# Optimization experiments

Measured on AMD Instinct MI355X. Metric: run time of the kernel, lower is better.

## Reference

```python
import jax, jax.numpy as jnp
import numpy as np

N_NODES = 50000
N_EDGES = 800000
N_INPUT = 512
N_HIDDEN = 64


def setup_inputs() -> dict:
    key = jax.random.key(0)
    ks = jax.random.split(key, 6)
    x = jax.random.normal(ks[0], (1, N_NODES, N_INPUT), dtype=jnp.float32)
    edge_rows = jax.random.randint(ks[1], (N_EDGES,), 0, N_NODES, dtype=jnp.int64)
    edge_cols = jax.random.randint(ks[2], (N_EDGES,), 0, N_NODES, dtype=jnp.int64)
    edge_vals = jax.random.uniform(ks[3], (N_EDGES,), dtype=jnp.float32)
    # xavier_normal_ on fc.weight: std = sqrt(2 / (fan_in + fan_out))
    std = float(np.sqrt(2.0 / (N_INPUT + N_HIDDEN)))
    W = jax.random.normal(ks[4], (N_HIDDEN, N_INPUT), dtype=jnp.float32) * std
    b = jnp.zeros((N_HIDDEN,), dtype=jnp.float32)
    alpha = jnp.full((1,), 0.25, dtype=jnp.float32)  # PReLU default init
    return {"x": x, "edge_rows": edge_rows, "edge_cols": edge_cols,
            "edge_vals": edge_vals, "W": W, "b": b, "alpha": alpha}


def reference(x, edge_rows, edge_cols, edge_vals, W, b, alpha):
    # Linear projection: [1, N, F_in] @ [F_in, F_out] -> [1, N, F_out]
    h = jnp.einsum('bnf,hf->bnh', x, W) + b
    h = jnp.squeeze(h, 0)  # [N, F_out]
    # spmm(adj, h): out[i] = sum_e vals[e] * h[cols[e]] for rows[e] == i
    msgs = edge_vals[:, None] * h[edge_cols]  # [E, F_out]
    agg = jax.ops.segment_sum(msgs, edge_rows, num_segments=N_NODES)  # [N, F_out]
    out = agg[None, :, :]  # [1, N, F_out]
    # PReLU with shared alpha
    return jnp.where(out >= 0, out, alpha * out)
```

## Files before the change

kernel.cpp:

```cpp
#include <hip/hip_runtime.h>

#define NODES 50000
#define NEDGES 800000
#define NIN 512
#define NHID 64

#define NB 391
#define BCAP 2560
#define EB 4096
#define NBA 196

#define XSTR 268

typedef __attribute__((ext_vector_type(8))) short short8v;
typedef __attribute__((ext_vector_type(8))) unsigned short ushort8v;
typedef __attribute__((ext_vector_type(4))) float f32x4;
typedef __attribute__((ext_vector_type(4))) unsigned int uint4v;

#define H_OFF    0
#define WBF_OFF  1600000
#define GCUR_OFF 1616384
#define RMETA_OFF 1616896
#define ECV2_OFF 1716896

__device__ inline unsigned short f2bf(float f) {
  unsigned u = __builtin_bit_cast(unsigned, f);
  u += 0x7FFF + ((u >> 16) & 1);
  return (unsigned short)(u >> 16);
}
__device__ inline float bf2f(unsigned short u) {
  return __builtin_bit_cast(float, (unsigned)u << 16);
}

__global__ __launch_bounds__(256) void init_kernel(
    const float* __restrict__ W, unsigned int* __restrict__ wbf,
    int* __restrict__ gcur)
{
  int i = blockIdx.x * 256 + threadIdx.x;
  if (i < NIN * NHID / 2) {
    float2 w = reinterpret_cast<const float2*>(W)[i];
    wbf[i] = (unsigned)f2bf(w.x) | ((unsigned)f2bf(w.y) << 16);
  }
  if (i < NB) gcur[i] = 0;
}

__global__ __launch_bounds__(256) void binA_kernel(
    const int* __restrict__ rows, const int* __restrict__ cols,
    const float* __restrict__ vals, int* __restrict__ gcur,
    int2* __restrict__ ecv2)
{
  __shared__ int hist[NB];
  __shared__ unsigned short slots[EB];
  int bid = blockIdx.x;
  int tid = (int)threadIdx.x;
  int e0 = bid * EB;

  for (int i = tid; i < NB; i += 256) hist[i] = 0;
  __syncthreads();
  #pragma unroll 4
  for (int k = 0; k < EB / 256; ++k) {
    int i = e0 + k * 256 + tid;
    if (i < NEDGES) {
      int r = rows[i];
      int s = atomicAdd(&hist[r >> 7], 1);
      slots[k * 256 + tid] = (unsigned short)s;
    }
  }
  __syncthreads();
  for (int i = tid; i < NB; i += 256) {
    int c = hist[i];
    hist[i] = c ? atomicAdd(&gcur[i], c) : 0;
  }
  __syncthreads();
  #pragma unroll 4
  for (int k = 0; k < EB / 256; ++k) {
    int i = e0 + k * 256 + tid;
    if (i < NEDGES) {
      int r = rows[i];
      int bkt = r >> 7;
      int sl = hist[bkt] + (int)slots[k * 256 + tid];
      if (sl < BCAP)
        ecv2[(long)bkt * BCAP + sl] =
            make_int2(cols[i] | ((r & 127) << 17), __float_as_int(vals[i]));
    }
  }
}

__global__ __launch_bounds__(256) void gemm_kernel(
    const float* __restrict__ x, const unsigned short* __restrict__ wbf,
    const float* __restrict__ b, unsigned short* __restrict__ h)
{
  __shared__ unsigned int xls[64 * XSTR];
  int blk = blockIdx.x;
  int tid = (int)threadIdx.x;

  #pragma unroll 8
  for (int c = 0; c < 32; ++c) {
    int idx = c * 256 + tid;
    int lrow = idx >> 7;
    int k4 = idx & 127;
    long grow = (long)blk * 64 + lrow;
    if (grow >= NODES) grow = NODES - 1;
    float4 v = *reinterpret_cast<const float4*>(x + grow * NIN + k4 * 4);
    unsigned lo, hi;
    asm("v_cvt_pk_bf16_f32 %0, %1, %2" : "=v"(lo) : "v"(v.x), "v"(v.y));
    asm("v_cvt_pk_bf16_f32 %0, %1, %2" : "=v"(hi) : "v"(v.z), "v"(v.w));
    *reinterpret_cast<uint2*>(&xls[lrow * XSTR + k4 * 2]) = make_uint2(lo, hi);
  }
  __syncthreads();

  int wv = tid >> 6;
  int lane = tid & 63;
  int r16 = lane & 15;
  int kg  = lane >> 4;
  int lrow = wv * 16 + r16;
  const unsigned int* rowp = &xls[lrow * XSTR];
  const unsigned short* wp = wbf + (long)r16 * NIN + kg * 8;

  f32x4 acc[4] = {{0,0,0,0},{0,0,0,0},{0,0,0,0},{0,0,0,0}};

  #pragma unroll
  for (int m = 0; m < 16; ++m) {
    uint4v ap = *reinterpret_cast<const uint4v*>(rowp + m * 16 + kg * 4);
    short8v af = __builtin_bit_cast(short8v, ap);
    #pragma unroll
    for (int ft = 0; ft < 4; ++ft) {
      short8v bfr = *reinterpret_cast<const short8v*>(
          wp + (long)ft * 16 * NIN + m * 32);
      acc[ft] = __builtin_amdgcn_mfma_f32_16x16x32_bf16(af, bfr, acc[ft], 0, 0, 0);
    }
  }

  int nbase = blk * 64 + wv * 16 + kg * 4;
  #pragma unroll
  for (int ft = 0; ft < 4; ++ft) {
    float bias = b[ft * 16 + r16];
    #pragma unroll
    for (int r = 0; r < 4; ++r) {
      int node = nbase + r;
      if (node < NODES)
        h[(long)node * NHID + ft * 16 + r16] = f2bf(acc[ft][r] + bias);
    }
  }
}

__global__ __launch_bounds__(256) void sortb_kernel(
    const int* __restrict__ gcur, int2* __restrict__ ecv2,
    int2* __restrict__ rowmeta)
{
  __shared__ int2 ed[BCAP];
  __shared__ unsigned short slots[BCAP];
  __shared__ int hist[128], base[128], stmp[128];
  int bkt = blockIdx.x;
  int tid = (int)threadIdx.x;

  int n = gcur[bkt];
  if (n > BCAP) n = BCAP;
  int2* bptr = ecv2 + (long)bkt * BCAP;

  if (tid < 128) hist[tid] = 0;
  __syncthreads();

  for (int i = tid; i < n; i += 256) {
    int2 e = bptr[i];
    ed[i] = e;
    int rl = e.x >> 17;
    slots[i] = (unsigned short)atomicAdd(&hist[rl], 1);
  }
  __syncthreads();

  int v = (tid < 128) ? hist[tid] : 0;
  if (tid < 128) stmp[tid] = v;
  __syncthreads();
  for (int d = 1; d < 128; d <<= 1) {
    int t = (tid < 128 && tid >= d) ? stmp[tid - d] : 0;
    __syncthreads();
    if (tid < 128) stmp[tid] += t;
    __syncthreads();
  }
  if (tid < 128) base[tid] = stmp[tid] - v;
  __syncthreads();

  for (int i = tid; i < n; i += 256) {
    int2 e = ed[i];
    int rl = e.x >> 17;
    int pos = base[rl] + (int)slots[i];
    bptr[pos] = make_int2(e.x & 0x1FFFF, e.y);
  }

  if (tid < 128) {
    int row = bkt * 128 + tid;
    if (row < NODES)
      rowmeta[row] = make_int2(bkt * BCAP + base[tid], hist[tid]);
  }
}

__global__ __launch_bounds__(256) void gather_kernel(
    const int2* __restrict__ rowmeta, const int2* __restrict__ ecv2,
    const unsigned short* __restrict__ h, const float* __restrict__ alpha,
    float* __restrict__ out)
{
  int wid = (int)((blockIdx.x * 256 + threadIdx.x) >> 6);
  if (wid >= NODES) return;
  int lane = (int)(threadIdx.x & 63);
  int eg = lane >> 3;
  int fo = lane & 7;
  int2 m = rowmeta[wid];
  int deg = m.y;
  const int2* base = ecv2 + m.x;
  float a = alpha[0];

  float acc[8] = {0.f, 0.f, 0.f, 0.f, 0.f, 0.f, 0.f, 0.f};
  int j = eg;
  int2 e = (j < deg) ? base[j] : make_int2(0, 0);
  while (j < deg) {
    int2 en = (j + 8 < deg) ? base[j + 8] : make_int2(0, 0);
    float v = __int_as_float(e.y);
    ushort8v hv = *reinterpret_cast<const ushort8v*>(&h[(long)e.x * NHID + fo * 8]);
    #pragma unroll
    for (int k = 0; k < 8; ++k)
      acc[k] = fmaf(v, bf2f(hv[k]), acc[k]);
    e = en;
    j += 8;
  }

  #pragma unroll
  for (int k = 0; k < 8; ++k) {
    acc[k] += __shfl_xor(acc[k], 8);
    acc[k] += __shfl_xor(acc[k], 16);
    acc[k] += __shfl_xor(acc[k], 32);
  }

  if (eg == 0) {
    float4 o0, o1;
    o0.x = acc[0] >= 0.f ? acc[0] : a * acc[0];
    o0.y = acc[1] >= 0.f ? acc[1] : a * acc[1];
    o0.z = acc[2] >= 0.f ? acc[2] : a * acc[2];
    o0.w = acc[3] >= 0.f ? acc[3] : a * acc[3];
    o1.x = acc[4] >= 0.f ? acc[4] : a * acc[4];
    o1.y = acc[5] >= 0.f ? acc[5] : a * acc[5];
    o1.z = acc[6] >= 0.f ? acc[6] : a * acc[6];
    o1.w = acc[7] >= 0.f ? acc[7] : a * acc[7];
    *reinterpret_cast<float4*>(&out[(long)wid * NHID + fo * 8]) = o0;
    *reinterpret_cast<float4*>(&out[(long)wid * NHID + fo * 8 + 4]) = o1;
  }
}

extern "C" void kernel_launch(void* const* d_in, const int* in_sizes, int n_in,
                              void* d_out, int out_size, void* d_ws, size_t ws_size,
                              hipStream_t stream) {
  const float* x     = (const float*)d_in[0];
  const int*   rows  = (const int*)d_in[1];
  const int*   cols  = (const int*)d_in[2];
  const float* vals  = (const float*)d_in[3];
  const float* W     = (const float*)d_in[4];
  const float* b     = (const float*)d_in[5];
  const float* alpha = (const float*)d_in[6];
  float* out = (float*)d_out;

  float* wsf = (float*)d_ws;
  unsigned short* h     = (unsigned short*)(wsf + H_OFF);
  unsigned int*   wbf   = (unsigned int*)(wsf + WBF_OFF);
  int*            gcur  = (int*)(wsf + GCUR_OFF);
  int2*           rmeta = (int2*)(wsf + RMETA_OFF);
  int2*           ecv2  = (int2*)(wsf + ECV2_OFF);

  init_kernel<<<64, 256, 0, stream>>>(W, wbf, gcur);
  binA_kernel<<<NBA, 256, 0, stream>>>(rows, cols, vals, gcur, ecv2);
  gemm_kernel<<<(NODES + 63) / 64, 256, 0, stream>>>(
      x, (const unsigned short*)wbf, b, h);
  sortb_kernel<<<NB, 256, 0, stream>>>(gcur, ecv2, rmeta);
  gather_kernel<<<NODES * 64 / 256, 256, 0, stream>>>(rmeta, ecv2, h, alpha, out);
}
```

Baseline: 107.1 us.

## Split GEMM K across waves with direct global loads and LDS reduction

The GEMM no longer stages a 64-row bf16 tile of x in LDS. Each 512-thread block now covers 32 rows, and its 8 waves split the K dimension four ways. Each wave loads x straight from global memory into registers, converts it to bf16 and feeds MFMA. Partial sums are reduced through a small LDS buffer before adding bias and storing. This removes the serial stage-then-compute barrier and raises parallelism, but adds an LDS reduction and uses narrower, less coalesced 32-byte-per-lane global reads.

```diff
diff --git a/kernel.cpp b/kernel.cpp
--- a/kernel.cpp
+++ b/kernel.cpp
@@ -9,8 +9,6 @@
 #define BCAP 2560
 #define EB 4096
 #define NBA 196
-
-#define XSTR 268
 
 typedef __attribute__((ext_vector_type(8))) short short8v;
 typedef __attribute__((ext_vector_type(8))) unsigned short ushort8v;
@@ -86,61 +84,69 @@
   }
 }
 
-__global__ __launch_bounds__(256) void gemm_kernel(
+__global__ __launch_bounds__(512) void gemm_kernel(
     const float* __restrict__ x, const unsigned short* __restrict__ wbf,
     const float* __restrict__ b, unsigned short* __restrict__ h)
 {
-  __shared__ unsigned int xls[64 * XSTR];
+  __shared__ float red[8][64][18];
   int blk = blockIdx.x;
   int tid = (int)threadIdx.x;
-
-  #pragma unroll 8
-  for (int c = 0; c < 32; ++c) {
-    int idx = c * 256 + tid;
-    int lrow = idx >> 7;
-    int k4 = idx & 127;
-    long grow = (long)blk * 64 + lrow;
-    if (grow >= NODES) grow = NODES - 1;
-    float4 v = *reinterpret_cast<const float4*>(x + grow * NIN + k4 * 4);
-    unsigned lo, hi;
-    asm("v_cvt_pk_bf16_f32 %0, %1, %2" : "=v"(lo) : "v"(v.x), "v"(v.y));
-    asm("v_cvt_pk_bf16_f32 %0, %1, %2" : "=v"(hi) : "v"(v.z), "v"(v.w));
-    *reinterpret_cast<uint2*>(&xls[lrow * XSTR + k4 * 2]) = make_uint2(lo, hi);
-  }
-  __syncthreads();
-
-  int wv = tid >> 6;
+  int w = tid >> 6;
   int lane = tid & 63;
+  int g  = w & 1;
+  int kc = w >> 1;
   int r16 = lane & 15;
   int kg  = lane >> 4;
-  int lrow = wv * 16 + r16;
-  const unsigned int* rowp = &xls[lrow * XSTR];
+
+  long row = (long)blk * 32 + g * 16 + r16;
+  if (row >= NODES) row = NODES - 1;
+  const float* xp = x + row * NIN + kg * 8;
   const unsigned short* wp = wbf + (long)r16 * NIN + kg * 8;
 
   f32x4 acc[4] = {{0,0,0,0},{0,0,0,0},{0,0,0,0},{0,0,0,0}};
 
   #pragma unroll
-  for (int m = 0; m < 16; ++m) {
-    uint4v ap = *reinterpret_cast<const uint4v*>(rowp + m * 16 + kg * 4);
+  for (int m = 0; m < 4; ++m) {
+    int M = kc * 4 + m;
+    float4 a0 = *reinterpret_cast<const float4*>(xp + M * 32);
+    float4 a1 = *reinterpret_cast<const float4*>(xp + M * 32 + 4);
+    unsigned q0, q1, q2, q3;
+    asm("v_cvt_pk_bf16_f32 %0, %1, %2" : "=v"(q0) : "v"(a0.x), "v"(a0.y));
+    asm("v_cvt_pk_bf16_f32 %0, %1, %2" : "=v"(q1) : "v"(a0.z), "v"(a0.w));
+    asm("v_cvt_pk_bf16_f32 %0, %1, %2" : "=v"(q2) : "v"(a1.x), "v"(a1.y));
+    asm("v_cvt_pk_bf16_f32 %0, %1, %2" : "=v"(q3) : "v"(a1.z), "v"(a1.w));
+    uint4v ap = {q0, q1, q2, q3};
     short8v af = __builtin_bit_cast(short8v, ap);
     #pragma unroll
     for (int ft = 0; ft < 4; ++ft) {
       short8v bfr = *reinterpret_cast<const short8v*>(
-          wp + (long)ft * 16 * NIN + m * 32);
+          wp + (long)ft * 16 * NIN + M * 32);
       acc[ft] = __builtin_amdgcn_mfma_f32_16x16x32_bf16(af, bfr, acc[ft], 0, 0, 0);
     }
   }
 
-  int nbase = blk * 64 + wv * 16 + kg * 4;
   #pragma unroll
   for (int ft = 0; ft < 4; ++ft) {
-    float bias = b[ft * 16 + r16];
-    #pragma unroll
-    for (int r = 0; r < 4; ++r) {
-      int node = nbase + r;
-      if (node < NODES)
-        h[(long)node * NHID + ft * 16 + r16] = f2bf(acc[ft][r] + bias);
-    }
+    *reinterpret_cast<float2*>(&red[w][lane][ft * 4]) =
+        make_float2(acc[ft][0], acc[ft][1]);
+    *reinterpret_cast<float2*>(&red[w][lane][ft * 4 + 2]) =
+        make_float2(acc[ft][2], acc[ft][3]);
+  }
+  __syncthreads();
+
+  #pragma unroll
+  for (int j = 0; j < 4; ++j) {
+    int o = tid * 4 + j;
+    int og  = o >> 10;
+    int ol  = (o >> 4) & 63;
+    int idx = o & 15;
+    float s = red[0 * 2 + og][ol][idx] + red[1 * 2 + og][ol][idx]
+            + red[2 * 2 + og][ol][idx] + red[3 * 2 + og][ol][idx];
+    int ft = idx >> 2, r = idx & 3;
+    int f = ft * 16 + (ol & 15);
+    long node = (long)blk * 32 + og * 16 + (ol >> 4) * 4 + r;
+    if (node < NODES)
+      h[node * NHID + f] = f2bf(s + b[f]);
   }
 }
 
@@ -267,7 +273,7 @@
 
   init_kernel<<<64, 256, 0, stream>>>(W, wbf, gcur);
   binA_kernel<<<NBA, 256, 0, stream>>>(rows, cols, vals, gcur, ecv2);
-  gemm_kernel<<<(NODES + 63) / 64, 256, 0, stream>>>(
+  gemm_kernel<<<(NODES + 31) / 32, 512, 0, stream>>>(
       x, (const unsigned short*)wbf, b, h);
   sortb_kernel<<<NB, 256, 0, stream>>>(gcur, ecv2, rmeta);
   gather_kernel<<<NODES * 64 / 256, 256, 0, stream>>>(rmeta, ecv2, h, alpha, out);
```

Result: faster. 99.82 us (-6.8%).
